# Performance work log

Hardware: AMD Instinct MI355X
Metric: run time of the kernel (lower is better)

## Reference

```python
import jax, jax.numpy as jnp
import numpy as np

N = 100000
E = 1600000
R = 8
DIN = 128
H = 128
C = 16
NROOT = 1024


def rgcn_conv(x, src, dst, edge_type, w_rel, w_root, bias):
    """PyG RGCNConv: per-relation mean aggregation + root weight + bias."""
    n, din = x.shape
    r = w_rel.shape[0]
    msgs = x[src]  # [E, din] gather
    seg = dst * r + edge_type  # combined (node, relation) segment id
    sums = jax.ops.segment_sum(msgs, seg, num_segments=n * r)        # [N*R, din]
    cnt = jax.ops.segment_sum(jnp.ones((msgs.shape[0],), x.dtype), seg,
                              num_segments=n * r)                    # [N*R]
    mean = sums / jnp.maximum(cnt, 1.0)[:, None]
    mean = mean.reshape(n, r, din)
    # relation-specific transform then sum over relations, plus root transform
    out = jnp.einsum('nrd,rde->ne', mean, w_rel) + x @ w_root + bias
    return out


def setup_inputs() -> dict:
    key = jax.random.key(0)
    ks = jax.random.split(key, 16)
    s = 0.05
    return {
        'x': jax.random.normal(ks[0], (N, DIN), jnp.float32),
        'edge_index': jax.random.randint(ks[1], (2, E), 0, N, jnp.int64),
        'edge_type': jax.random.randint(ks[2], (E,), 0, R, jnp.int64),
        'root_idx': jax.random.randint(ks[3], (NROOT,), 0, N, jnp.int64),
        'wrel1': jax.random.normal(ks[4], (R, DIN, H), jnp.float32) * s,
        'root1': jax.random.normal(ks[5], (DIN, H), jnp.float32) * s,
        'b1': jax.random.normal(ks[6], (H,), jnp.float32) * s,
        'wrel2': jax.random.normal(ks[7], (R, H, H), jnp.float32) * s,
        'root2': jax.random.normal(ks[8], (H, H), jnp.float32) * s,
        'b2': jax.random.normal(ks[9], (H,), jnp.float32) * s,
        'wrel3': jax.random.normal(ks[10], (R, H, C), jnp.float32) * s,
        'root3': jax.random.normal(ks[11], (H, C), jnp.float32) * s,
        'b3': jax.random.normal(ks[12], (C,), jnp.float32) * s,
    }


def reference(x, edge_index, edge_type, root_idx,
              wrel1, root1, b1, wrel2, root2, b2, wrel3, root3, b3):
    src, dst = edge_index[0], edge_index[1]
    h = jax.nn.relu(rgcn_conv(x, src, dst, edge_type, wrel1, root1, b1))
    # hidden conv (relu; dropout is identity in eval mode)
    h = jax.nn.relu(rgcn_conv(h, src, dst, edge_type, wrel2, root2, b2))
    # final conv, no activation
    h = rgcn_conv(h, src, dst, edge_type, wrel3, root3, b3)
    return h[root_idx]  # [NROOT, C]
```

## Files before the change

kernel.cpp:

```cpp
#include <hip/hip_runtime.h>
#include <hip/hip_fp16.h>


typedef _Float16 f16;
typedef _Float16 f16x2 __attribute__((ext_vector_type(2)));
typedef _Float16 f16x4 __attribute__((ext_vector_type(4)));
typedef _Float16 f16x8 __attribute__((ext_vector_type(8)));
typedef float f32x4 __attribute__((ext_vector_type(4)));

#define NREL 8
#define ACHUNK 8192
#define WTELEM (640 * 128)

__global__ void k_hist(const int* __restrict__ dst, int E, int* __restrict__ cnt) {
  int e = blockIdx.x * 256 + threadIdx.x;
  if (e < E) atomicAdd(&cnt[dst[e]], 1);
}

__global__ void k_scan1(const int* __restrict__ in, int* __restrict__ out,
                        int* __restrict__ part, int n) {
  __shared__ int sh[256];
  int b = blockIdx.x, t = threadIdx.x;
  int base = b * 4096 + t * 16;
  int v[16]; int s = 0;
#pragma unroll
  for (int j = 0; j < 16; j++) { int idx = base + j; int x = (idx < n) ? in[idx] : 0; v[j] = s; s += x; }
  sh[t] = s; __syncthreads();
  for (int off = 1; off < 256; off <<= 1) {
    int x = 0; if (t >= off) x = sh[t - off];
    __syncthreads();
    if (t >= off) sh[t] += x;
    __syncthreads();
  }
  int excl = (t == 0) ? 0 : sh[t - 1];
  if (t == 255) part[b] = sh[255];
#pragma unroll
  for (int j = 0; j < 16; j++) { int idx = base + j; if (idx < n) out[idx] = v[j] + excl; }
}

__global__ void k_scan2(int* __restrict__ part, int nb) {
  __shared__ int sh[256];
  int t = threadIdx.x;
  sh[t] = (t < nb) ? part[t] : 0; __syncthreads();
  for (int off = 1; off < 256; off <<= 1) {
    int x = 0; if (t >= off) x = sh[t - off];
    __syncthreads();
    if (t >= off) sh[t] += x;
    __syncthreads();
  }
  if (t < nb) part[t] = (t == 0) ? 0 : sh[t - 1];
}

__global__ void k_scan3(int* __restrict__ out, const int* __restrict__ part, int n) {
  int i = blockIdx.x * 256 + threadIdx.x;
  if (i < n) out[i] += part[i >> 12];
}

__global__ void k_scatter(const int* __restrict__ src, const int* __restrict__ dstv,
                          const int* __restrict__ et, int E,
                          const int* __restrict__ off, int* __restrict__ fill,
                          int* __restrict__ sps) {
  int e = blockIdx.x * 256 + threadIdx.x;
  if (e >= E) return;
  int d = dstv[e];
  int pos = off[d] + atomicAdd(&fill[d], 1);
  sps[pos] = src[e] | (et[e] << 20);
}

__global__ __launch_bounds__(256) void k_sinvp(const int* __restrict__ sps,
                                               const int* __restrict__ off,
                                               float* __restrict__ sinvp, int N) {
  __shared__ int c[16][8];
  int t = threadIdx.x;
  int g = t >> 4, st = t & 15;
  int n = blockIdx.x * 16 + g;
  if (st < 8) c[g][st] = 0;
  __syncthreads();
  if (n < N) {
    int e0 = off[n], e1 = off[n + 1];
    for (int e = e0 + st; e < e1; e += 16)
      atomicAdd(&c[g][((unsigned)sps[e]) >> 20], 1);
  }
  __syncthreads();
  if (n < N && st < 8) {
    int cc = c[g][st];
    sinvp[n * 8 + st] = 1.0f / (float)(cc > 1 ? cc : 1);
  }
}

__global__ void k_sentinel(int* __restrict__ p, int v) { *p = v; }

__global__ __launch_bounds__(256) void k_bhist(const int* __restrict__ dstv, int E,
                                               int* __restrict__ bcnt, int nbuck) {
  __shared__ int h[512];
  int t = threadIdx.x;
  for (int i = t; i < 512; i += 256) h[i] = 0;
  __syncthreads();
  int lo = blockIdx.x * ACHUNK;
  int hi = lo + ACHUNK < E ? lo + ACHUNK : E;
  for (int e = lo + t; e < hi; e += 256) atomicAdd(&h[dstv[e] >> 8], 1);
  __syncthreads();
  for (int i = t; i < nbuck; i += 256)
    if (h[i]) atomicAdd(&bcnt[i], h[i]);
}

__global__ __launch_bounds__(512) void k_bscan(const int* __restrict__ bcnt,
                                               int* __restrict__ boff, int nbuck) {
  __shared__ int sh[512];
  int t = threadIdx.x;
  sh[t] = (t < nbuck) ? bcnt[t] : 0;
  __syncthreads();
  for (int o = 1; o < 512; o <<= 1) {
    int v = 0; if (t >= o) v = sh[t - o];
    __syncthreads();
    sh[t] += v;
    __syncthreads();
  }
  if (t <= nbuck && t < 512) boff[t] = (t == 0) ? 0 : sh[t - 1];
  if (t == 511 && nbuck >= 512) boff[nbuck] = sh[511];
}

__global__ __launch_bounds__(256) void k_bucketA(
    const int* __restrict__ src, const int* __restrict__ dstv,
    const int* __restrict__ et, int E, const int* __restrict__ boff,
    int* __restrict__ bfill, int* __restrict__ tmp, int nbuck) {
  __shared__ int hist[512];
  __shared__ int base[512];
  int t = threadIdx.x;
  int lo = blockIdx.x * ACHUNK;
  int hi = lo + ACHUNK < E ? lo + ACHUNK : E;
  for (int i = t; i < nbuck; i += 256) hist[i] = 0;
  __syncthreads();
  for (int e = lo + t; e < hi; e += 256)
    atomicAdd(&hist[dstv[e] >> 8], 1);
  __syncthreads();
  for (int i = t; i < nbuck; i += 256) {
    int c = hist[i];
    base[i] = c ? (boff[i] + atomicAdd(&bfill[i], c)) : 0;
  }
  __syncthreads();
  for (int e = lo + t; e < hi; e += 256) {
    int d = dstv[e];
    int b = d >> 8;
    int pos = atomicAdd(&base[b], 1);
    tmp[pos] = src[e] | (et[e] << 20) | ((d & 255) << 23);
  }
}

__global__ __launch_bounds__(256) void k_bucketB3(const int* __restrict__ tmp,
                                                  const int* __restrict__ boff,
                                                  int* __restrict__ off,
                                                  int* __restrict__ sps,
                                                  float* __restrict__ sinvp, int N) {
  __shared__ int cty[2048];
  __shared__ int sh[256];
  __shared__ int loff[257];
  __shared__ int fill[256];
  int b = blockIdx.x, t = threadIdx.x;
  int n0 = b << 8;
  int nn = (N - n0) < 256 ? (N - n0) : 256;
#pragma unroll
  for (int j = 0; j < 8; j++) cty[t + j * 256] = 0;
  __syncthreads();
  int e0 = boff[b], e1 = boff[b + 1];
  for (int e = e0 + t; e < e1; e += 256) {
    int v = tmp[e];
    int dl = (v >> 23) & 255, ty = (v >> 20) & 7;
    atomicAdd(&cty[dl * 8 + ty], 1);
  }
  __syncthreads();
  {
    int c = 0;
#pragma unroll
    for (int j = 0; j < 8; j++) c += cty[t * 8 + j];
    sh[t] = c;
  }
  __syncthreads();
  for (int o = 1; o < 256; o <<= 1) {
    int v = 0; if (t >= o) v = sh[t - o];
    __syncthreads();
    sh[t] += v;
    __syncthreads();
  }
  loff[t] = (t == 0) ? 0 : sh[t - 1];
  if (t == 255) loff[256] = sh[255];
  __syncthreads();
  if (t < nn) off[n0 + t] = e0 + loff[t];
  for (int i = t; i < 2048; i += 256) {
    int n = n0 + (i >> 3);
    if (n < N) {
      int c = cty[i];
      sinvp[(size_t)n * 8 + (i & 7)] = 1.0f / (float)(c > 1 ? c : 1);
    }
  }
  fill[t] = 0;
  __syncthreads();
  for (int e = e0 + t; e < e1; e += 256) {
    int v = tmp[e];
    int dl = (v >> 23) & 255;
    int pos = e0 + loff[dl] + atomicAdd(&fill[dl], 1);
    sps[pos] = v & 0x7FFFFF;
  }
}

__global__ void k_mark(const int* __restrict__ ridx, const int* __restrict__ off,
                       const int* __restrict__ sps, int* __restrict__ mark) {
  int i = blockIdx.x, t = threadIdx.x;
  int n = ridx[i];
  if (t == 0) mark[n] = 1;
  int e0 = off[n], e1 = off[n + 1];
  for (int e = e0 + t; e < e1; e += 64) mark[sps[e] & 0xFFFFF] = 1;
}

__global__ void k_tpw4(const float* __restrict__ wrel1, const float* __restrict__ root1,
                       const float* __restrict__ wrel2, const float* __restrict__ root2,
                       f16* __restrict__ Wt, int PW, int npass) {
  int row = blockIdx.x, k = threadIdx.x, q = blockIdx.y;
  int layer = q / npass, p = q - layer * npass;
  const float* wrel = layer ? wrel2 : wrel1;
  const float* wroot = layer ? root2 : root1;
  float v = 0.f;
  if (row < 9 * PW) {
    int cb = row / PW, j = row - cb * PW;
    int col = p * PW + j;
    v = (cb < 8) ? wrel[(size_t)cb * 16384 + k * 128 + col] : wroot[k * 128 + col];
  }
  Wt[(size_t)q * WTELEM + (size_t)row * 128 + k] = (f16)v;
}

template <typename AT>
__global__ __launch_bounds__(256) void k_gemm3(const AT* __restrict__ A,
                                               const f16* __restrict__ Bt,
                                               f16* __restrict__ Y, int M, int ncol) {
  __shared__ f16 As[128 * 136];
  int tid = threadIdx.x;
  int m0 = blockIdx.x * 128;
  int PW = ncol / 9;
  int cbs = (PW == 64) ? 6 : 5;
#pragma unroll
  for (int cch = 0; cch < 8; cch++) {
    int ci = tid + cch * 256;
    int row = ci >> 4, c8 = ci & 15;
    int gm = m0 + row;
    f16x8 va = {};
    if (gm < M) {
      if constexpr (sizeof(AT) == 2) {
        va = *(const f16x8*)((const f16*)A + (size_t)gm * 128 + c8 * 8);
      } else {
        const float4* ap = (const float4*)((const float*)A + (size_t)gm * 128);
        float4 u0 = ap[c8 * 2], u1 = ap[c8 * 2 + 1];
        va[0] = (f16)u0.x; va[1] = (f16)u0.y; va[2] = (f16)u0.z; va[3] = (f16)u0.w;
        va[4] = (f16)u1.x; va[5] = (f16)u1.y; va[6] = (f16)u1.z; va[7] = (f16)u1.w;
      }
    }
    *(f16x8*)(As + row * 136 + c8 * 8) = va;
  }
  __syncthreads();
  int wid = tid >> 6, lane = tid & 63;
  int wm = (wid & 1) * 64, wn = (wid >> 1) * 64;
  int lm = lane & 15, lk = lane >> 4;
  f16x8 af[4][4];
#pragma unroll
  for (int ks = 0; ks < 4; ks++)
#pragma unroll
    for (int i = 0; i < 4; i++)
      af[ks][i] = *(const f16x8*)(As + (wm + i * 16 + lm) * 136 + ks * 32 + lk * 8);
  __syncthreads();
  f16* H = As;
  int NT = (ncol + 127) >> 7;
  for (int nt = blockIdx.y; nt < NT; nt += gridDim.y) {
    int n0 = nt * 128;
    f32x4 acc[4][4] = {};
#pragma unroll
    for (int ks = 0; ks < 4; ks++) {
      f16x8 b[4];
#pragma unroll
      for (int j = 0; j < 4; j++)
        b[j] = *(const f16x8*)(Bt + (size_t)(n0 + wn + j * 16 + lm) * 128 + ks * 32 + lk * 8);
#pragma unroll
      for (int i = 0; i < 4; i++)
#pragma unroll
        for (int j = 0; j < 4; j++)
          acc[i][j] = __builtin_amdgcn_mfma_f32_16x16x32_f16(b[j], af[ks][i], acc[i][j], 0, 0, 0);
    }
#pragma unroll
    for (int i = 0; i < 4; i++)
#pragma unroll
      for (int j = 0; j < 4; j++) {
        f16x4 o;
        o[0] = (f16)acc[i][j][0]; o[1] = (f16)acc[i][j][1];
        o[2] = (f16)acc[i][j][2]; o[3] = (f16)acc[i][j][3];
        *(f16x4*)(H + (wm + i * 16 + lm) * 136 + wn + j * 16 + lk * 4) = o;
      }
    __syncthreads();
    for (int i = tid; i < 128 * 16; i += 256) {
      int row = i >> 4, c8 = i & 15;
      int gm = m0 + row;
      int gc = n0 + c8 * 8;
      if (gm < M && gc < ncol) {
        int cb = gc >> cbs, wi = gc & (PW - 1);
        *(f16x8*)(Y + ((size_t)cb * M + gm) * PW + wi) =
            *(const f16x8*)(H + row * 136 + c8 * 8);
      }
    }
    __syncthreads();
  }
}

template <int PW>
__global__ __launch_bounds__(256) void k_edge_v(
    const f16* __restrict__ Y, const int* __restrict__ sps,
    const int* __restrict__ off, const float* __restrict__ sinvp,
    const float* __restrict__ bias, f16* __restrict__ hout,
    const int* __restrict__ mark, int N, int pass) {
  constexpr int CPL = PW / 16;
  int t = threadIdx.x;
  int g = t >> 4, st = t & 15;
  int n = blockIdx.x * 16 + g;
  if (n >= N) return;
  if (mark && !mark[n]) return;
  float sv = (st < 8) ? sinvp[n * 8 + st] : 0.f;
  int e0 = off[n], e1 = off[n + 1];
  float a[CPL], b2[CPL];
  {
    const f16* rp = Y + ((size_t)8 * N + n) * PW + st * CPL;
    const float* bp = bias + pass * PW + st * CPL;
#pragma unroll
    for (int q = 0; q < CPL; q++) { a[q] = (float)rp[q] + bp[q]; b2[q] = 0.f; }
  }
  int sgbase = t & 48;
  int e = e0;
  for (; e + 1 < e1; e += 2) {
    int p0 = sps[e], p1 = sps[e + 1];
    int s0 = p0 & 0xFFFFF, ty0 = ((unsigned)p0) >> 20;
    int s1 = p1 & 0xFFFFF, ty1 = ((unsigned)p1) >> 20;
    float sc0 = __shfl(sv, sgbase | ty0);
    float sc1 = __shfl(sv, sgbase | ty1);
    const f16* q0 = Y + ((size_t)ty0 * N + s0) * PW + st * CPL;
    const f16* q1 = Y + ((size_t)ty1 * N + s1) * PW + st * CPL;
    if constexpr (PW == 64) {
      f16x4 v0 = *(const f16x4*)q0;
      f16x4 v1 = *(const f16x4*)q1;
      a[0] += (float)v0[0] * sc0; a[1] += (float)v0[1] * sc0;
      a[2] += (float)v0[2] * sc0; a[3] += (float)v0[3] * sc0;
      b2[0] += (float)v1[0] * sc1; b2[1] += (float)v1[1] * sc1;
      b2[2] += (float)v1[2] * sc1; b2[3] += (float)v1[3] * sc1;
    } else {
      f16x2 v0 = *(const f16x2*)q0;
      f16x2 v1 = *(const f16x2*)q1;
      a[0] += (float)v0[0] * sc0; a[1] += (float)v0[1] * sc0;
      b2[0] += (float)v1[0] * sc1; b2[1] += (float)v1[1] * sc1;
    }
  }
  if (e < e1) {
    int p0 = sps[e];
    int s0 = p0 & 0xFFFFF, ty0 = ((unsigned)p0) >> 20;
    float sc0 = __shfl(sv, sgbase | ty0);
    const f16* q0 = Y + ((size_t)ty0 * N + s0) * PW + st * CPL;
    if constexpr (PW == 64) {
      f16x4 v0 = *(const f16x4*)q0;
      a[0] += (float)v0[0] * sc0; a[1] += (float)v0[1] * sc0;
      a[2] += (float)v0[2] * sc0; a[3] += (float)v0[3] * sc0;
    } else {
      f16x2 v0 = *(const f16x2*)q0;
      a[0] += (float)v0[0] * sc0; a[1] += (float)v0[1] * sc0;
    }
  }
  if constexpr (PW == 64) {
    f16x4 o;
#pragma unroll
    for (int q = 0; q < 4; q++) o[q] = (f16)fmaxf(a[q] + b2[q], 0.f);
    *(f16x4*)(hout + (size_t)n * 128 + pass * PW + st * 4) = o;
  } else {
    f16x2 o;
#pragma unroll
    for (int q = 0; q < 2; q++) o[q] = (f16)fmaxf(a[q] + b2[q], 0.f);
    *(f16x2*)(hout + (size_t)n * 128 + pass * PW + st * 2) = o;
  }
}

__global__ __launch_bounds__(128) void k_layer3(const f16* __restrict__ h2,
                                                const int* __restrict__ sps,
                                                const int* __restrict__ off,
                                                const float* __restrict__ sinvp,
                                                const int* __restrict__ ridx,
                                                const float* __restrict__ wrel,
                                                const float* __restrict__ wroot,
                                                const float* __restrict__ b3,
                                                float* __restrict__ out) {
  __shared__ f16 W[9 * 2048];
  __shared__ float red[2][16];
  __shared__ float sinv_s[8];
  int t = threadIdx.x;
  int n = ridx[blockIdx.x];
  for (int j = t; j < 9 * 2048; j += 128)
    W[j] = (f16)((j < 8 * 2048) ? wrel[j] : wroot[j - 8 * 2048]);
  if (t < 8) sinv_s[t] = sinvp[n * 8 + t];
  __syncthreads();
  int e0 = off[n], e1 = off[n + 1];
  int c = t & 15, kg = t >> 4;
  float a = 0.f;
  for (int e = e0; e < e1; e++) {
    int ps = sps[e];
    int s = ps & 0xFFFFF, ty = ((unsigned)ps) >> 20;
    float p = 0.f;
#pragma unroll
    for (int j = 0; j < 16; j++) {
      int k = kg * 16 + j;
      p += (float)h2[(size_t)s * 128 + k] * (float)W[ty * 2048 + k * 16 + c];
    }
    a += sinv_s[ty] * p;
  }
  {
    float p = 0.f;
#pragma unroll
    for (int j = 0; j < 16; j++) {
      int k = kg * 16 + j;
      p += (float)h2[(size_t)n * 128 + k] * (float)W[8 * 2048 + k * 16 + c];
    }
    a += p;
  }
  a += __shfl_xor(a, 16);
  a += __shfl_xor(a, 32);
  if ((t & 63) < 16) red[t >> 6][t & 15] = a;
  __syncthreads();
  if (t < 16) out[(size_t)blockIdx.x * 16 + t] = red[0][t] + red[1][t] + b3[t];
}

extern "C" void kernel_launch(void* const* d_in, const int* in_sizes, int n_in,
                              void* d_out, int out_size, void* d_ws, size_t ws_size,
                              hipStream_t stream) {
  const float* x     = (const float*)d_in[0];
  const int*   eidx  = (const int*)d_in[1];
  const int*   etyp  = (const int*)d_in[2];
  const int*   ridx  = (const int*)d_in[3];
  const float* wrel1 = (const float*)d_in[4];
  const float* root1 = (const float*)d_in[5];
  const float* b1    = (const float*)d_in[6];
  const float* wrel2 = (const float*)d_in[7];
  const float* root2 = (const float*)d_in[8];
  const float* b2    = (const float*)d_in[9];
  const float* wrel3 = (const float*)d_in[10];
  const float* root3 = (const float*)d_in[11];
  const float* b3    = (const float*)d_in[12];

  int N = in_sizes[0] / 128;
  int E = in_sizes[2];
  int NROOT = in_sizes[3];
  const int* esrc = eidx;
  const int* edst = eidx + E;

  char* p = (char*)d_ws;
  auto alloc = [&](size_t bytes) { void* r = (void*)p; p += (bytes + 255) & ~(size_t)255; return r; };
  int*   off   = (int*)alloc((size_t)(N + 1) * 4);
  int*   sps   = (int*)alloc((size_t)E * 4);
  f16*   h1    = (f16*)alloc((size_t)N * 128 * 2);
  f16*   h2    = (f16*)alloc((size_t)N * 128 * 2);
  int*   mark  = (int*)alloc((size_t)N * 4);
  float* sinvp = (float*)alloc((size_t)N * 8 * 4);
  f16*   Wt    = (f16*)alloc((size_t)WTELEM * 2 * 8);
  int*   bcnt  = (int*)alloc(512 * 4);
  int*   boff  = (int*)alloc(513 * 4);
  int*   bfill = (int*)alloc(512 * 4);

  size_t used = (size_t)(p - (char*)d_ws);
  size_t remain = ws_size > used ? ws_size - used : 0;
  int PW = (remain >= (size_t)N * 9 * 64 * 2 + (1u << 20)) ? 64 : 32;
  int ldy = 9 * PW;
  f16* Y = (f16*)alloc((size_t)N * ldy * 2);
  int* tmp  = (int*)Y;
  int* part = tmp + E;
  int* fill = part + 4096;

  int nbuck = (N + 255) >> 8;
  int nbA = (E + ACHUNK - 1) / ACHUNK;
  int npass = 128 / PW;
  int NT = (ldy + 127) / 128;
  hipMemsetAsync(mark, 0, (size_t)N * 4, stream);
  k_tpw4<<<dim3(NT * 128, 2 * npass), 128, 0, stream>>>(wrel1, root1, wrel2, root2,
                                                        Wt, PW, npass);

  if (nbuck <= 512) {
    hipMemsetAsync(bcnt, 0, 512 * 4, stream);
    hipMemsetAsync(bfill, 0, 512 * 4, stream);
    k_bhist<<<nbA, 256, 0, stream>>>(edst, E, bcnt, nbuck);
    k_bscan<<<1, 512, 0, stream>>>(bcnt, boff, nbuck);
    k_bucketA<<<nbA, 256, 0, stream>>>(esrc, edst, etyp, E, boff, bfill, tmp, nbuck);
    k_bucketB3<<<nbuck, 256, 0, stream>>>(tmp, boff, off, sps, sinvp, N);
    k_sentinel<<<1, 1, 0, stream>>>(off + N, E);
  } else {
    int eb = (E + 255) / 256;
    hipMemsetAsync(off, 0, (size_t)(N + 1) * 4, stream);
    hipMemsetAsync(fill, 0, (size_t)N * 4, stream);
    k_hist<<<eb, 256, 0, stream>>>(edst, E, off);
    int nb1 = (N + 4095) / 4096;
    k_scan1<<<nb1, 256, 0, stream>>>(off, off, part, N);
    k_scan2<<<1, 256, 0, stream>>>(part, nb1);
    k_scan3<<<(N + 255) / 256, 256, 0, stream>>>(off, part, N);
    k_sentinel<<<1, 1, 0, stream>>>(off + N, E);
    k_scatter<<<eb, 256, 0, stream>>>(esrc, edst, etyp, E, off, fill, sps);
    int ng16f = (N + 15) / 16;
    k_sinvp<<<ng16f, 256, 0, stream>>>(sps, off, sinvp, N);
  }
  k_mark<<<NROOT, 64, 0, stream>>>(ridx, off, sps, mark);
  int ng16 = (N + 15) / 16;

  int mb = (N + 127) / 128;

  for (int ps = 0; ps < npass; ps++) {
    k_gemm3<float><<<dim3(mb, 2), 256, 0, stream>>>(x, Wt + (size_t)ps * WTELEM, Y, N, ldy);
    if (PW == 64)
      k_edge_v<64><<<ng16, 256, 0, stream>>>(Y, sps, off, sinvp, b1, h1, nullptr, N, ps);
    else
      k_edge_v<32><<<ng16, 256, 0, stream>>>(Y, sps, off, sinvp, b1, h1, nullptr, N, ps);
  }
  for (int ps = 0; ps < npass; ps++) {
    k_gemm3<f16><<<dim3(mb, 2), 256, 0, stream>>>(h1, Wt + (size_t)(npass + ps) * WTELEM,
                                                  Y, N, ldy);
    if (PW == 64)
      k_edge_v<64><<<ng16, 256, 0, stream>>>(Y, sps, off, sinvp, b2, h2, mark, N, ps);
    else
      k_edge_v<32><<<ng16, 256, 0, stream>>>(Y, sps, off, sinvp, b2, h2, mark, N, ps);
  }
  k_layer3<<<NROOT, 128, 0, stream>>>(h2, sps, off, sinvp, ridx, wrel3, root3, b3,
                                      (float*)d_out);
}
```

Measured before the change: 476.0 us.

## Compact layer-2 to marked nodes with aggregate-then-transform GEMM

Layer 2 no longer runs a full N-row transform GEMM followed by an edge pass that discards unmarked nodes. The marked node set (roots plus their neighbours) is compacted into a list, their per-relation means are aggregated from h1, and a small GEMM over the compacted rows produces h2 only for those nodes. Layer 3 reads through the compacted index. This cuts layer-2 work to about 16K nodes, at the cost of an atomic compaction pass and a capacity bound on the compact buffer.

New measurement: 446.2 us. -6.3%, faster.

```diff
diff --git a/kernel.cpp b/kernel.cpp
--- a/kernel.cpp
+++ b/kernel.cpp
@@ -212,20 +212,35 @@
   for (int e = e0 + t; e < e1; e += 64) mark[sps[e] & 0xFFFFF] = 1;
 }
 
+__global__ void k_compact(const int* __restrict__ mark, int* __restrict__ midx,
+                          int* __restrict__ mlist, int* __restrict__ nm, int N) {
+  int n = blockIdx.x * 256 + threadIdx.x;
+  if (n < N && mark[n]) {
+    int i = atomicAdd(nm, 1);
+    midx[n] = i;
+    mlist[i] = n;
+  }
+}
+
 __global__ void k_tpw4(const float* __restrict__ wrel1, const float* __restrict__ root1,
-                       const float* __restrict__ wrel2, const float* __restrict__ root2,
-                       f16* __restrict__ Wt, int PW, int npass) {
+                       f16* __restrict__ Wt, int PW) {
   int row = blockIdx.x, k = threadIdx.x, q = blockIdx.y;
-  int layer = q / npass, p = q - layer * npass;
-  const float* wrel = layer ? wrel2 : wrel1;
-  const float* wroot = layer ? root2 : root1;
   float v = 0.f;
   if (row < 9 * PW) {
     int cb = row / PW, j = row - cb * PW;
-    int col = p * PW + j;
-    v = (cb < 8) ? wrel[(size_t)cb * 16384 + k * 128 + col] : wroot[k * 128 + col];
+    int col = q * PW + j;
+    v = (cb < 8) ? wrel1[(size_t)cb * 16384 + k * 128 + col] : root1[k * 128 + col];
   }
   Wt[(size_t)q * WTELEM + (size_t)row * 128 + k] = (f16)v;
+}
+
+__global__ void k_tpwc2(const float* __restrict__ wrel2, const float* __restrict__ root2,
+                        f16* __restrict__ Wc) {
+  int c = blockIdx.x, k = threadIdx.x;
+#pragma unroll
+  for (int r = 0; r < 8; r++)
+    Wc[(size_t)c * 1152 + r * 128 + k] = (f16)wrel2[(size_t)r * 16384 + k * 128 + c];
+  Wc[(size_t)c * 1152 + 1024 + k] = (f16)root2[(size_t)k * 128 + c];
 }
 
 template <typename AT>
@@ -311,14 +326,12 @@
 __global__ __launch_bounds__(256) void k_edge_v(
     const f16* __restrict__ Y, const int* __restrict__ sps,
     const int* __restrict__ off, const float* __restrict__ sinvp,
-    const float* __restrict__ bias, f16* __restrict__ hout,
-    const int* __restrict__ mark, int N, int pass) {
+    const float* __restrict__ bias, f16* __restrict__ hout, int N, int pass) {
   constexpr int CPL = PW / 16;
   int t = threadIdx.x;
   int g = t >> 4, st = t & 15;
   int n = blockIdx.x * 16 + g;
   if (n >= N) return;
-  if (mark && !mark[n]) return;
   float sv = (st < 8) ? sinvp[n * 8 + st] : 0.f;
   int e0 = off[n], e1 = off[n + 1];
   float a[CPL], b2[CPL];
@@ -379,15 +392,120 @@
   }
 }
 
-__global__ __launch_bounds__(128) void k_layer3(const f16* __restrict__ h2,
-                                                const int* __restrict__ sps,
-                                                const int* __restrict__ off,
-                                                const float* __restrict__ sinvp,
-                                                const int* __restrict__ ridx,
-                                                const float* __restrict__ wrel,
-                                                const float* __restrict__ wroot,
-                                                const float* __restrict__ b3,
-                                                float* __restrict__ out) {
+__global__ __launch_bounds__(128) void k_agg2(
+    const f16* __restrict__ h1, const int* __restrict__ sps,
+    const int* __restrict__ off, const float* __restrict__ sinvp,
+    const int* __restrict__ mlist, const int* __restrict__ nm_p,
+    f16* __restrict__ Mc, int cap) {
+  int nm = *nm_p; if (nm > cap) nm = cap;
+  int t = threadIdx.x;
+  for (int i = blockIdx.x; i < nm; i += gridDim.x) {
+    int n = mlist[i];
+    int e0 = off[n], e1 = off[n + 1];
+    float acc[8];
+#pragma unroll
+    for (int r = 0; r < 8; r++) acc[r] = 0.f;
+    int e = e0;
+    for (; e + 1 < e1; e += 2) {
+      int p0 = sps[e], p1 = sps[e + 1];
+      int s0 = p0 & 0xFFFFF, ty0 = ((unsigned)p0) >> 20;
+      int s1 = p1 & 0xFFFFF, ty1 = ((unsigned)p1) >> 20;
+      float v0 = (float)h1[(size_t)s0 * 128 + t];
+      float v1 = (float)h1[(size_t)s1 * 128 + t];
+#pragma unroll
+      for (int r = 0; r < 8; r++) {
+        acc[r] += (ty0 == r) ? v0 : 0.f;
+        acc[r] += (ty1 == r) ? v1 : 0.f;
+      }
+    }
+    if (e < e1) {
+      int p0 = sps[e];
+      int s0 = p0 & 0xFFFFF, ty0 = ((unsigned)p0) >> 20;
+      float v0 = (float)h1[(size_t)s0 * 128 + t];
+#pragma unroll
+      for (int r = 0; r < 8; r++) acc[r] += (ty0 == r) ? v0 : 0.f;
+    }
+    f16* mp = Mc + (size_t)i * 1152;
+#pragma unroll
+    for (int r = 0; r < 8; r++)
+      mp[r * 128 + t] = (f16)(acc[r] * sinvp[(size_t)n * 8 + r]);
+    mp[1024 + t] = h1[(size_t)n * 128 + t];
+  }
+}
+
+__global__ __launch_bounds__(256) void k_gemm_c(const f16* __restrict__ Mc,
+                                                const f16* __restrict__ Wc,
+                                                const float* __restrict__ bias,
+                                                const int* __restrict__ nm_p,
+                                                f16* __restrict__ h2c, int cap) {
+  int nm = *nm_p; if (nm > cap) nm = cap;
+  int m0 = blockIdx.x * 128;
+  if (m0 >= nm) return;
+  __shared__ f16 As[128 * 136];
+  int tid = threadIdx.x;
+  int wid = tid >> 6, lane = tid & 63;
+  int wm = (wid & 1) * 64, wn = (wid >> 1) * 64;
+  int lm = lane & 15, lk = lane >> 4;
+  f32x4 acc[4][4] = {};
+  for (int kc = 0; kc < 9; kc++) {
+    __syncthreads();
+#pragma unroll
+    for (int cch = 0; cch < 8; cch++) {
+      int ci = tid + cch * 256;
+      int row = ci >> 4, c8 = ci & 15;
+      int gm = m0 + row;
+      f16x8 va = {};
+      if (gm < nm) va = *(const f16x8*)(Mc + (size_t)gm * 1152 + kc * 128 + c8 * 8);
+      *(f16x8*)(As + row * 136 + c8 * 8) = va;
+    }
+    __syncthreads();
+#pragma unroll
+    for (int ks = 0; ks < 4; ks++) {
+      f16x8 a[4], b[4];
+#pragma unroll
+      for (int j = 0; j < 4; j++)
+        b[j] = *(const f16x8*)(Wc + (size_t)(wn + j * 16 + lm) * 1152 + kc * 128 + ks * 32 + lk * 8);
+#pragma unroll
+      for (int i = 0; i < 4; i++)
+        a[i] = *(const f16x8*)(As + (wm + i * 16 + lm) * 136 + ks * 32 + lk * 8);
+#pragma unroll
+      for (int i = 0; i < 4; i++)
+#pragma unroll
+        for (int j = 0; j < 4; j++)
+          acc[i][j] = __builtin_amdgcn_mfma_f32_16x16x32_f16(b[j], a[i], acc[i][j], 0, 0, 0);
+    }
+  }
+  __syncthreads();
+  f16* H = As;
+#pragma unroll
+  for (int i = 0; i < 4; i++)
+#pragma unroll
+    for (int j = 0; j < 4; j++) {
+      f16x4 o;
+#pragma unroll
+      for (int q = 0; q < 4; q++)
+        o[q] = (f16)fmaxf(acc[i][j][q] + bias[wn + j * 16 + lk * 4 + q], 0.f);
+      *(f16x4*)(H + (wm + i * 16 + lm) * 136 + wn + j * 16 + lk * 4) = o;
+    }
+  __syncthreads();
+  for (int i = tid; i < 128 * 16; i += 256) {
+    int row = i >> 4, c8 = i & 15;
+    int gm = m0 + row;
+    if (gm < nm)
+      *(f16x8*)(h2c + (size_t)gm * 128 + c8 * 8) = *(const f16x8*)(H + row * 136 + c8 * 8);
+  }
+}
+
+__global__ __launch_bounds__(128) void k_layer3c(const f16* __restrict__ h2c,
+                                                 const int* __restrict__ midx,
+                                                 const int* __restrict__ sps,
+                                                 const int* __restrict__ off,
+                                                 const float* __restrict__ sinvp,
+                                                 const int* __restrict__ ridx,
+                                                 const float* __restrict__ wrel,
+                                                 const float* __restrict__ wroot,
+                                                 const float* __restrict__ b3,
+                                                 float* __restrict__ out) {
   __shared__ f16 W[9 * 2048];
   __shared__ float red[2][16];
   __shared__ float sinv_s[8];
@@ -403,20 +521,22 @@
   for (int e = e0; e < e1; e++) {
     int ps = sps[e];
     int s = ps & 0xFFFFF, ty = ((unsigned)ps) >> 20;
+    int si = midx[s];
     float p = 0.f;
 #pragma unroll
     for (int j = 0; j < 16; j++) {
       int k = kg * 16 + j;
-      p += (float)h2[(size_t)s * 128 + k] * (float)W[ty * 2048 + k * 16 + c];
+      p += (float)h2c[(size_t)si * 128 + k] * (float)W[ty * 2048 + k * 16 + c];
     }
     a += sinv_s[ty] * p;
   }
   {
+    int ni = midx[n];
     float p = 0.f;
 #pragma unroll
     for (int j = 0; j < 16; j++) {
       int k = kg * 16 + j;
-      p += (float)h2[(size_t)n * 128 + k] * (float)W[8 * 2048 + k * 16 + c];
+      p += (float)h2c[(size_t)ni * 128 + k] * (float)W[8 * 2048 + k * 16 + c];
     }
     a += p;
   }
@@ -455,10 +575,14 @@
   int*   off   = (int*)alloc((size_t)(N + 1) * 4);
   int*   sps   = (int*)alloc((size_t)E * 4);
   f16*   h1    = (f16*)alloc((size_t)N * 128 * 2);
-  f16*   h2    = (f16*)alloc((size_t)N * 128 * 2);
+  f16*   h2c   = (f16*)alloc((size_t)N * 128 * 2);
   int*   mark  = (int*)alloc((size_t)N * 4);
+  int*   midx  = (int*)alloc((size_t)N * 4);
+  int*   mlist = (int*)alloc((size_t)N * 4);
+  int*   nmv   = (int*)alloc(256);
   float* sinvp = (float*)alloc((size_t)N * 8 * 4);
-  f16*   Wt    = (f16*)alloc((size_t)WTELEM * 2 * 8);
+  f16*   Wt    = (f16*)alloc((size_t)WTELEM * 2 * 4);
+  f16*   Wc    = (f16*)alloc((size_t)128 * 1152 * 2);
   int*   bcnt  = (int*)alloc(512 * 4);
   int*   boff  = (int*)alloc(513 * 4);
   int*   bfill = (int*)alloc(512 * 4);
@@ -471,14 +595,17 @@
   int* tmp  = (int*)Y;
   int* part = tmp + E;
   int* fill = part + 4096;
+  f16* Mc   = Y;
+  int  cap  = (int)(((size_t)N * ldy) / 1152);
 
   int nbuck = (N + 255) >> 8;
   int nbA = (E + ACHUNK - 1) / ACHUNK;
   int npass = 128 / PW;
   int NT = (ldy + 127) / 128;
   hipMemsetAsync(mark, 0, (size_t)N * 4, stream);
-  k_tpw4<<<dim3(NT * 128, 2 * npass), 128, 0, stream>>>(wrel1, root1, wrel2, root2,
-                                                        Wt, PW, npass);
+  hipMemsetAsync(nmv, 0, 256, stream);
+  k_tpw4<<<dim3(NT * 128, npass), 128, 0, stream>>>(wrel1, root1, Wt, PW);
+  k_tpwc2<<<128, 128, 0, stream>>>(wrel2, root2, Wc);
 
   if (nbuck <= 512) {
     hipMemsetAsync(bcnt, 0, 512 * 4, stream);
@@ -503,6 +630,7 @@
     k_sinvp<<<ng16f, 256, 0, stream>>>(sps, off, sinvp, N);
   }
   k_mark<<<NROOT, 64, 0, stream>>>(ridx, off, sps, mark);
+  k_compact<<<(N + 255) / 256, 256, 0, stream>>>(mark, midx, mlist, nmv, N);
   int ng16 = (N + 15) / 16;
 
   int mb = (N + 127) / 128;
@@ -510,18 +638,12 @@
   for (int ps = 0; ps < npass; ps++) {
     k_gemm3<float><<<dim3(mb, 2), 256, 0, stream>>>(x, Wt + (size_t)ps * WTELEM, Y, N, ldy);
     if (PW == 64)
-      k_edge_v<64><<<ng16, 256, 0, stream>>>(Y, sps, off, sinvp, b1, h1, nullptr, N, ps);
+      k_edge_v<64><<<ng16, 256, 0, stream>>>(Y, sps, off, sinvp, b1, h1, N, ps);
     else
-      k_edge_v<32><<<ng16, 256, 0, stream>>>(Y, sps, off, sinvp, b1, h1, nullptr, N, ps);
-  }
-  for (int ps = 0; ps < npass; ps++) {
-    k_gemm3<f16><<<dim3(mb, 2), 256, 0, stream>>>(h1, Wt + (size_t)(npass + ps) * WTELEM,
-                                                  Y, N, ldy);
-    if (PW == 64)
-      k_edge_v<64><<<ng16, 256, 0, stream>>>(Y, sps, off, sinvp, b2, h2, mark, N, ps);
-    else
-      k_edge_v<32><<<ng16, 256, 0, stream>>>(Y, sps, off, sinvp, b2, h2, mark, N, ps);
-  }
-  k_layer3<<<NROOT, 128, 0, stream>>>(h2, sps, off, sinvp, ridx, wrel3, root3, b3,
-                                      (float*)d_out);
-}
+      k_edge_v<32><<<ng16, 256, 0, stream>>>(Y, sps, off, sinvp, b1, h1, N, ps);
+  }
+  k_agg2<<<2048, 128, 0, stream>>>(h1, sps, off, sinvp, mlist, nmv, Mc, cap);
+  k_gemm_c<<<(cap + 127) / 128, 256, 0, stream>>>(Mc, Wc, b2, nmv, h2c, cap);
+  k_layer3c<<<NROOT, 128, 0, stream>>>(h2c, midx, sps, off, sinvp, ridx, wrel3, root3,
+                                       b3, (float*)d_out);
+}
```

## Aggregate-then-transform RGCN layers with compacted layer-2 node set

Applied to the files above, without the earlier changes.

Replaces transform-then-gather (GEMM producing 9 relation projections per node, then an edge gather over 64/32-column passes) with gathering raw 128-dim features per relation into a mean buffer, then a single K=1152 GEMM fused with bias and ReLU. Layer 2 is computed only for compacted marked nodes (roots and their neighbours) through an index list, and layer 3 reads the compact h2. It also casts x to fp16 once and merges the memsets into one init kernel. The scalar per-thread 128-wide gather and an atomic-based compaction order are new costs, and the large per-node mean buffer is chunked by workspace capacity.

After: 631.2 us. +32.6%, slower.

```diff
diff --git a/kernel.cpp b/kernel.cpp
--- a/kernel.cpp
+++ b/kernel.cpp
@@ -3,14 +3,12 @@
 
 
 typedef _Float16 f16;
-typedef _Float16 f16x2 __attribute__((ext_vector_type(2)));
 typedef _Float16 f16x4 __attribute__((ext_vector_type(4)));
 typedef _Float16 f16x8 __attribute__((ext_vector_type(8)));
 typedef float f32x4 __attribute__((ext_vector_type(4)));
 
 #define NREL 8
 #define ACHUNK 8192
-#define WTELEM (640 * 128)
 
 __global__ void k_hist(const int* __restrict__ dst, int E, int* __restrict__ cnt) {
   int e = blockIdx.x * 256 + threadIdx.x;
@@ -89,6 +87,14 @@
 }
 
 __global__ void k_sentinel(int* __restrict__ p, int v) { *p = v; }
+
+__global__ void k_init(int* __restrict__ bcnt, int* __restrict__ bfill,
+                       int* __restrict__ nmv, int* __restrict__ mark, int N) {
+  int i = blockIdx.x * 256 + threadIdx.x;
+  if (i < 512) { bcnt[i] = 0; bfill[i] = 0; }
+  if (i < 64) nmv[i] = 0;
+  if (i < N) mark[i] = 0;
+}
 
 __global__ __launch_bounds__(256) void k_bhist(const int* __restrict__ dstv, int E,
                                                int* __restrict__ bcnt, int nbuck) {
@@ -212,182 +218,162 @@
   for (int e = e0 + t; e < e1; e += 64) mark[sps[e] & 0xFFFFF] = 1;
 }
 
-__global__ void k_tpw4(const float* __restrict__ wrel1, const float* __restrict__ root1,
-                       const float* __restrict__ wrel2, const float* __restrict__ root2,
-                       f16* __restrict__ Wt, int PW, int npass) {
-  int row = blockIdx.x, k = threadIdx.x, q = blockIdx.y;
-  int layer = q / npass, p = q - layer * npass;
-  const float* wrel = layer ? wrel2 : wrel1;
-  const float* wroot = layer ? root2 : root1;
-  float v = 0.f;
-  if (row < 9 * PW) {
-    int cb = row / PW, j = row - cb * PW;
-    int col = p * PW + j;
-    v = (cb < 8) ? wrel[(size_t)cb * 16384 + k * 128 + col] : wroot[k * 128 + col];
-  }
-  Wt[(size_t)q * WTELEM + (size_t)row * 128 + k] = (f16)v;
-}
-
-template <typename AT>
-__global__ __launch_bounds__(256) void k_gemm3(const AT* __restrict__ A,
-                                               const f16* __restrict__ Bt,
-                                               f16* __restrict__ Y, int M, int ncol) {
+__global__ void k_compact(const int* __restrict__ mark, int* __restrict__ midx,
+                          int* __restrict__ mlist, int* __restrict__ nm, int N) {
+  int n = blockIdx.x * 256 + threadIdx.x;
+  if (n < N && mark[n]) {
+    int i = atomicAdd(nm, 1);
+    midx[n] = i;
+    mlist[i] = n;
+  }
+}
+
+__global__ void k_f32_to_f16(const float* __restrict__ in, f16* __restrict__ out, int n4) {
+  int i = blockIdx.x * 256 + threadIdx.x;
+  if (i < n4) {
+    float4 v = ((const float4*)in)[i];
+    f16x4 o; o[0] = (f16)v.x; o[1] = (f16)v.y; o[2] = (f16)v.z; o[3] = (f16)v.w;
+    ((f16x4*)out)[i] = o;
+  }
+}
+
+__global__ void k_tpwc(const float* __restrict__ wrel, const float* __restrict__ wroot,
+                       f16* __restrict__ Wc) {
+  int c = blockIdx.x, k = threadIdx.x;
+#pragma unroll
+  for (int r = 0; r < 8; r++)
+    Wc[(size_t)c * 1152 + r * 128 + k] = (f16)wrel[(size_t)r * 16384 + k * 128 + c];
+  Wc[(size_t)c * 1152 + 1024 + k] = (f16)wroot[(size_t)k * 128 + c];
+}
+
+__global__ __launch_bounds__(128) void k_agg(
+    const f16* __restrict__ h, const int* __restrict__ sps,
+    const int* __restrict__ off, const float* __restrict__ sinvp,
+    const int* __restrict__ mlist, const int* __restrict__ nm_p,
+    int cnt, int nbase, f16* __restrict__ Mc) {
+  int nm = cnt;
+  if (nm_p) { int v = *nm_p; if (v < nm) nm = v; }
+  int t = threadIdx.x;
+  for (int i = blockIdx.x; i < nm; i += gridDim.x) {
+    int n = mlist ? mlist[i] : (nbase + i);
+    int e0 = off[n], e1 = off[n + 1];
+    float acc[8];
+#pragma unroll
+    for (int r = 0; r < 8; r++) acc[r] = 0.f;
+    int e = e0;
+    for (; e + 3 < e1; e += 4) {
+      int p0 = sps[e], p1 = sps[e + 1], p2 = sps[e + 2], p3 = sps[e + 3];
+      float v0 = (float)h[(size_t)(p0 & 0xFFFFF) * 128 + t];
+      float v1 = (float)h[(size_t)(p1 & 0xFFFFF) * 128 + t];
+      float v2 = (float)h[(size_t)(p2 & 0xFFFFF) * 128 + t];
+      float v3 = (float)h[(size_t)(p3 & 0xFFFFF) * 128 + t];
+      int ty0 = ((unsigned)p0) >> 20, ty1 = ((unsigned)p1) >> 20;
+      int ty2 = ((unsigned)p2) >> 20, ty3 = ((unsigned)p3) >> 20;
+#pragma unroll
+      for (int r = 0; r < 8; r++) {
+        acc[r] += (ty0 == r) ? v0 : 0.f;
+        acc[r] += (ty1 == r) ? v1 : 0.f;
+        acc[r] += (ty2 == r) ? v2 : 0.f;
+        acc[r] += (ty3 == r) ? v3 : 0.f;
+      }
+    }
+    for (; e < e1; e++) {
+      int p0 = sps[e];
+      float v0 = (float)h[(size_t)(p0 & 0xFFFFF) * 128 + t];
+      int ty0 = ((unsigned)p0) >> 20;
+#pragma unroll
+      for (int r = 0; r < 8; r++) acc[r] += (ty0 == r) ? v0 : 0.f;
+    }
+    f16* mp = Mc + (size_t)i * 1024;
+#pragma unroll
+    for (int r = 0; r < 8; r++)
+      mp[r * 128 + t] = (f16)(acc[r] * sinvp[(size_t)n * 8 + r]);
+  }
+}
+
+__global__ __launch_bounds__(256) void k_gemm_c(const f16* __restrict__ Mc,
+                                                const f16* __restrict__ rootsrc,
+                                                const int* __restrict__ ml,
+                                                const f16* __restrict__ Wc,
+                                                const float* __restrict__ bias,
+                                                const int* __restrict__ nm_p,
+                                                int cnt, f16* __restrict__ out) {
+  int nm = cnt;
+  if (nm_p) { int v = *nm_p; if (v < nm) nm = v; }
+  int m0 = blockIdx.x * 128;
+  if (m0 >= nm) return;
   __shared__ f16 As[128 * 136];
   int tid = threadIdx.x;
-  int m0 = blockIdx.x * 128;
-  int PW = ncol / 9;
-  int cbs = (PW == 64) ? 6 : 5;
-#pragma unroll
-  for (int cch = 0; cch < 8; cch++) {
-    int ci = tid + cch * 256;
-    int row = ci >> 4, c8 = ci & 15;
-    int gm = m0 + row;
-    f16x8 va = {};
-    if (gm < M) {
-      if constexpr (sizeof(AT) == 2) {
-        va = *(const f16x8*)((const f16*)A + (size_t)gm * 128 + c8 * 8);
-      } else {
-        const float4* ap = (const float4*)((const float*)A + (size_t)gm * 128);
-        float4 u0 = ap[c8 * 2], u1 = ap[c8 * 2 + 1];
-        va[0] = (f16)u0.x; va[1] = (f16)u0.y; va[2] = (f16)u0.z; va[3] = (f16)u0.w;
-        va[4] = (f16)u1.x; va[5] = (f16)u1.y; va[6] = (f16)u1.z; va[7] = (f16)u1.w;
-      }
-    }
-    *(f16x8*)(As + row * 136 + c8 * 8) = va;
-  }
-  __syncthreads();
   int wid = tid >> 6, lane = tid & 63;
   int wm = (wid & 1) * 64, wn = (wid >> 1) * 64;
   int lm = lane & 15, lk = lane >> 4;
-  f16x8 af[4][4];
-#pragma unroll
-  for (int ks = 0; ks < 4; ks++)
-#pragma unroll
-    for (int i = 0; i < 4; i++)
-      af[ks][i] = *(const f16x8*)(As + (wm + i * 16 + lm) * 136 + ks * 32 + lk * 8);
+  f32x4 acc[4][4] = {};
+  for (int kc = 0; kc < 9; kc++) {
+    __syncthreads();
+#pragma unroll
+    for (int cch = 0; cch < 8; cch++) {
+      int ci = tid + cch * 256;
+      int row = ci >> 4, c8 = ci & 15;
+      int gm = m0 + row;
+      f16x8 va = {};
+      if (gm < nm) {
+        if (kc < 8) {
+          va = *(const f16x8*)(Mc + (size_t)gm * 1024 + kc * 128 + c8 * 8);
+        } else {
+          int rn = ml ? ml[gm] : gm;
+          va = *(const f16x8*)(rootsrc + (size_t)rn * 128 + c8 * 8);
+        }
+      }
+      *(f16x8*)(As + row * 136 + c8 * 8) = va;
+    }
+    __syncthreads();
+#pragma unroll
+    for (int ks = 0; ks < 4; ks++) {
+      f16x8 a[4], b[4];
+#pragma unroll
+      for (int j = 0; j < 4; j++)
+        b[j] = *(const f16x8*)(Wc + (size_t)(wn + j * 16 + lm) * 1152 + kc * 128 + ks * 32 + lk * 8);
+#pragma unroll
+      for (int i = 0; i < 4; i++)
+        a[i] = *(const f16x8*)(As + (wm + i * 16 + lm) * 136 + ks * 32 + lk * 8);
+#pragma unroll
+      for (int i = 0; i < 4; i++)
+#pragma unroll
+        for (int j = 0; j < 4; j++)
+          acc[i][j] = __builtin_amdgcn_mfma_f32_16x16x32_f16(b[j], a[i], acc[i][j], 0, 0, 0);
+    }
+  }
   __syncthreads();
   f16* H = As;
-  int NT = (ncol + 127) >> 7;
-  for (int nt = blockIdx.y; nt < NT; nt += gridDim.y) {
-    int n0 = nt * 128;
-    f32x4 acc[4][4] = {};
-#pragma unroll
-    for (int ks = 0; ks < 4; ks++) {
-      f16x8 b[4];
-#pragma unroll
-      for (int j = 0; j < 4; j++)
-        b[j] = *(const f16x8*)(Bt + (size_t)(n0 + wn + j * 16 + lm) * 128 + ks * 32 + lk * 8);
-#pragma unroll
-      for (int i = 0; i < 4; i++)
-#pragma unroll
-        for (int j = 0; j < 4; j++)
-          acc[i][j] = __builtin_amdgcn_mfma_f32_16x16x32_f16(b[j], af[ks][i], acc[i][j], 0, 0, 0);
-    }
-#pragma unroll
-    for (int i = 0; i < 4; i++)
-#pragma unroll
-      for (int j = 0; j < 4; j++) {
-        f16x4 o;
-        o[0] = (f16)acc[i][j][0]; o[1] = (f16)acc[i][j][1];
-        o[2] = (f16)acc[i][j][2]; o[3] = (f16)acc[i][j][3];
-        *(f16x4*)(H + (wm + i * 16 + lm) * 136 + wn + j * 16 + lk * 4) = o;
-      }
-    __syncthreads();
-    for (int i = tid; i < 128 * 16; i += 256) {
-      int row = i >> 4, c8 = i & 15;
-      int gm = m0 + row;
-      int gc = n0 + c8 * 8;
-      if (gm < M && gc < ncol) {
-        int cb = gc >> cbs, wi = gc & (PW - 1);
-        *(f16x8*)(Y + ((size_t)cb * M + gm) * PW + wi) =
-            *(const f16x8*)(H + row * 136 + c8 * 8);
-      }
-    }
-    __syncthreads();
-  }
-}
-
-template <int PW>
-__global__ __launch_bounds__(256) void k_edge_v(
-    const f16* __restrict__ Y, const int* __restrict__ sps,
-    const int* __restrict__ off, const float* __restrict__ sinvp,
-    const float* __restrict__ bias, f16* __restrict__ hout,
-    const int* __restrict__ mark, int N, int pass) {
-  constexpr int CPL = PW / 16;
-  int t = threadIdx.x;
-  int g = t >> 4, st = t & 15;
-  int n = blockIdx.x * 16 + g;
-  if (n >= N) return;
-  if (mark && !mark[n]) return;
-  float sv = (st < 8) ? sinvp[n * 8 + st] : 0.f;
-  int e0 = off[n], e1 = off[n + 1];
-  float a[CPL], b2[CPL];
-  {
-    const f16* rp = Y + ((size_t)8 * N + n) * PW + st * CPL;
-    const float* bp = bias + pass * PW + st * CPL;
-#pragma unroll
-    for (int q = 0; q < CPL; q++) { a[q] = (float)rp[q] + bp[q]; b2[q] = 0.f; }
-  }
-  int sgbase = t & 48;
-  int e = e0;
-  for (; e + 1 < e1; e += 2) {
-    int p0 = sps[e], p1 = sps[e + 1];
-    int s0 = p0 & 0xFFFFF, ty0 = ((unsigned)p0) >> 20;
-    int s1 = p1 & 0xFFFFF, ty1 = ((unsigned)p1) >> 20;
-    float sc0 = __shfl(sv, sgbase | ty0);
-    float sc1 = __shfl(sv, sgbase | ty1);
-    const f16* q0 = Y + ((size_t)ty0 * N + s0) * PW + st * CPL;
-    const f16* q1 = Y + ((size_t)ty1 * N + s1) * PW + st * CPL;
-    if constexpr (PW == 64) {
-      f16x4 v0 = *(const f16x4*)q0;
-      f16x4 v1 = *(const f16x4*)q1;
-      a[0] += (float)v0[0] * sc0; a[1] += (float)v0[1] * sc0;
-      a[2] += (float)v0[2] * sc0; a[3] += (float)v0[3] * sc0;
-      b2[0] += (float)v1[0] * sc1; b2[1] += (float)v1[1] * sc1;
-      b2[2] += (float)v1[2] * sc1; b2[3] += (float)v1[3] * sc1;
-    } else {
-      f16x2 v0 = *(const f16x2*)q0;
-      f16x2 v1 = *(const f16x2*)q1;
-      a[0] += (float)v0[0] * sc0; a[1] += (float)v0[1] * sc0;
-      b2[0] += (float)v1[0] * sc1; b2[1] += (float)v1[1] * sc1;
-    }
-  }
-  if (e < e1) {
-    int p0 = sps[e];
-    int s0 = p0 & 0xFFFFF, ty0 = ((unsigned)p0) >> 20;
-    float sc0 = __shfl(sv, sgbase | ty0);
-    const f16* q0 = Y + ((size_t)ty0 * N + s0) * PW + st * CPL;
-    if constexpr (PW == 64) {
-      f16x4 v0 = *(const f16x4*)q0;
-      a[0] += (float)v0[0] * sc0; a[1] += (float)v0[1] * sc0;
-      a[2] += (float)v0[2] * sc0; a[3] += (float)v0[3] * sc0;
-    } else {
-      f16x2 v0 = *(const f16x2*)q0;
-      a[0] += (float)v0[0] * sc0; a[1] += (float)v0[1] * sc0;
-    }
-  }
-  if constexpr (PW == 64) {
-    f16x4 o;
-#pragma unroll
-    for (int q = 0; q < 4; q++) o[q] = (f16)fmaxf(a[q] + b2[q], 0.f);
-    *(f16x4*)(hout + (size_t)n * 128 + pass * PW + st * 4) = o;
-  } else {
-    f16x2 o;
-#pragma unroll
-    for (int q = 0; q < 2; q++) o[q] = (f16)fmaxf(a[q] + b2[q], 0.f);
-    *(f16x2*)(hout + (size_t)n * 128 + pass * PW + st * 2) = o;
-  }
-}
-
-__global__ __launch_bounds__(128) void k_layer3(const f16* __restrict__ h2,
-                                                const int* __restrict__ sps,
-                                                const int* __restrict__ off,
-                                                const float* __restrict__ sinvp,
-                                                const int* __restrict__ ridx,
-                                                const float* __restrict__ wrel,
-                                                const float* __restrict__ wroot,
-                                                const float* __restrict__ b3,
-                                                float* __restrict__ out) {
+#pragma unroll
+  for (int i = 0; i < 4; i++)
+#pragma unroll
+    for (int j = 0; j < 4; j++) {
+      f16x4 o;
+#pragma unroll
+      for (int q = 0; q < 4; q++)
+        o[q] = (f16)fmaxf(acc[i][j][q] + bias[wn + j * 16 + lk * 4 + q], 0.f);
+      *(f16x4*)(H + (wm + i * 16 + lm) * 136 + wn + j * 16 + lk * 4) = o;
+    }
+  __syncthreads();
+  for (int i = tid; i < 128 * 16; i += 256) {
+    int row = i >> 4, c8 = i & 15;
+    int gm = m0 + row;
+    if (gm < nm)
+      *(f16x8*)(out + (size_t)gm * 128 + c8 * 8) = *(const f16x8*)(H + row * 136 + c8 * 8);
+  }
+}
+
+__global__ __launch_bounds__(128) void k_layer3c(const f16* __restrict__ h2c,
+                                                 const int* __restrict__ midx,
+                                                 const int* __restrict__ sps,
+                                                 const int* __restrict__ off,
+                                                 const float* __restrict__ sinvp,
+                                                 const int* __restrict__ ridx,
+                                                 const float* __restrict__ wrel,
+                                                 const float* __restrict__ wroot,
+                                                 const float* __restrict__ b3,
+                                                 float* __restrict__ out) {
   __shared__ f16 W[9 * 2048];
   __shared__ float red[2][16];
   __shared__ float sinv_s[8];
@@ -403,20 +389,22 @@
   for (int e = e0; e < e1; e++) {
     int ps = sps[e];
     int s = ps & 0xFFFFF, ty = ((unsigned)ps) >> 20;
+    int si = midx[s];
     float p = 0.f;
 #pragma unroll
     for (int j = 0; j < 16; j++) {
       int k = kg * 16 + j;
-      p += (float)h2[(size_t)s * 128 + k] * (float)W[ty * 2048 + k * 16 + c];
+      p += (float)h2c[(size_t)si * 128 + k] * (float)W[ty * 2048 + k * 16 + c];
     }
     a += sinv_s[ty] * p;
   }
   {
+    int ni = midx[n];
     float p = 0.f;
 #pragma unroll
     for (int j = 0; j < 16; j++) {
       int k = kg * 16 + j;
-      p += (float)h2[(size_t)n * 128 + k] * (float)W[8 * 2048 + k * 16 + c];
+      p += (float)h2c[(size_t)ni * 128 + k] * (float)W[8 * 2048 + k * 16 + c];
     }
     a += p;
   }
@@ -455,34 +443,38 @@
   int*   off   = (int*)alloc((size_t)(N + 1) * 4);
   int*   sps   = (int*)alloc((size_t)E * 4);
   f16*   h1    = (f16*)alloc((size_t)N * 128 * 2);
-  f16*   h2    = (f16*)alloc((size_t)N * 128 * 2);
+  f16*   h2c   = (f16*)alloc((size_t)N * 128 * 2);
   int*   mark  = (int*)alloc((size_t)N * 4);
+  int*   midx  = (int*)alloc((size_t)N * 4);
+  int*   mlist = (int*)alloc((size_t)N * 4);
+  int*   nmv   = (int*)alloc(256);
   float* sinvp = (float*)alloc((size_t)N * 8 * 4);
-  f16*   Wt    = (f16*)alloc((size_t)WTELEM * 2 * 8);
+  f16*   Wc1   = (f16*)alloc((size_t)128 * 1152 * 2);
+  f16*   Wc2   = (f16*)alloc((size_t)128 * 1152 * 2);
   int*   bcnt  = (int*)alloc(512 * 4);
   int*   boff  = (int*)alloc(513 * 4);
   int*   bfill = (int*)alloc(512 * 4);
 
   size_t used = (size_t)(p - (char*)d_ws);
   size_t remain = ws_size > used ? ws_size - used : 0;
-  int PW = (remain >= (size_t)N * 9 * 64 * 2 + (1u << 20)) ? 64 : 32;
-  int ldy = 9 * PW;
-  f16* Y = (f16*)alloc((size_t)N * ldy * 2);
-  int* tmp  = (int*)Y;
+  char* scratch = (char*)alloc(0);
+  int cap = (int)(remain / 2048);
+  if (cap > N) cap = N;
+  if (cap < 128) cap = 128;
+  int* tmp  = (int*)scratch;
   int* part = tmp + E;
   int* fill = part + 4096;
+  f16* Mc   = (f16*)scratch;
 
   int nbuck = (N + 255) >> 8;
   int nbA = (E + ACHUNK - 1) / ACHUNK;
-  int npass = 128 / PW;
-  int NT = (ldy + 127) / 128;
-  hipMemsetAsync(mark, 0, (size_t)N * 4, stream);
-  k_tpw4<<<dim3(NT * 128, 2 * npass), 128, 0, stream>>>(wrel1, root1, wrel2, root2,
-                                                        Wt, PW, npass);
+  k_init<<<(N + 255) / 256, 256, 0, stream>>>(bcnt, bfill, nmv, mark, N);
+  k_tpwc<<<128, 128, 0, stream>>>(wrel1, root1, Wc1);
+  k_tpwc<<<128, 128, 0, stream>>>(wrel2, root2, Wc2);
+  f16* xh = h2c;
+  k_f32_to_f16<<<((N * 32) + 255) / 256, 256, 0, stream>>>(x, xh, N * 32);
 
   if (nbuck <= 512) {
-    hipMemsetAsync(bcnt, 0, 512 * 4, stream);
-    hipMemsetAsync(bfill, 0, 512 * 4, stream);
     k_bhist<<<nbA, 256, 0, stream>>>(edst, E, bcnt, nbuck);
     k_bscan<<<1, 512, 0, stream>>>(bcnt, boff, nbuck);
     k_bucketA<<<nbA, 256, 0, stream>>>(esrc, edst, etyp, E, boff, bfill, tmp, nbuck);
@@ -503,25 +495,17 @@
     k_sinvp<<<ng16f, 256, 0, stream>>>(sps, off, sinvp, N);
   }
   k_mark<<<NROOT, 64, 0, stream>>>(ridx, off, sps, mark);
-  int ng16 = (N + 15) / 16;
-
-  int mb = (N + 127) / 128;
-
-  for (int ps = 0; ps < npass; ps++) {
-    k_gemm3<float><<<dim3(mb, 2), 256, 0, stream>>>(x, Wt + (size_t)ps * WTELEM, Y, N, ldy);
-    if (PW == 64)
-      k_edge_v<64><<<ng16, 256, 0, stream>>>(Y, sps, off, sinvp, b1, h1, nullptr, N, ps);
-    else
-      k_edge_v<32><<<ng16, 256, 0, stream>>>(Y, sps, off, sinvp, b1, h1, nullptr, N, ps);
-  }
-  for (int ps = 0; ps < npass; ps++) {
-    k_gemm3<f16><<<dim3(mb, 2), 256, 0, stream>>>(h1, Wt + (size_t)(npass + ps) * WTELEM,
-                                                  Y, N, ldy);
-    if (PW == 64)
-      k_edge_v<64><<<ng16, 256, 0, stream>>>(Y, sps, off, sinvp, b2, h2, mark, N, ps);
-    else
-      k_edge_v<32><<<ng16, 256, 0, stream>>>(Y, sps, off, sinvp, b2, h2, mark, N, ps);
-  }
-  k_layer3<<<NROOT, 128, 0, stream>>>(h2, sps, off, sinvp, ridx, wrel3, root3, b3,
-                                      (float*)d_out);
-}
+  k_compact<<<(N + 255) / 256, 256, 0, stream>>>(mark, midx, mlist, nmv, N);
+
+  for (int m0 = 0; m0 < N; m0 += cap) {
+    int cnt = (N - m0) < cap ? (N - m0) : cap;
+    k_agg<<<2048, 128, 0, stream>>>(xh, sps, off, sinvp, nullptr, nullptr, cnt, m0, Mc);
+    k_gemm_c<<<(cnt + 127) / 128, 256, 0, stream>>>(Mc, xh + (size_t)m0 * 128, nullptr,
+                                                    Wc1, b1, nullptr, cnt,
+                                                    h1 + (size_t)m0 * 128);
+  }
+  k_agg<<<2048, 128, 0, stream>>>(h1, sps, off, sinvp, mlist, nmv, cap, 0, Mc);
+  k_gemm_c<<<(cap + 127) / 128, 256, 0, stream>>>(Mc, h1, mlist, Wc2, b2, nmv, cap, h2c);
+  k_layer3c<<<NROOT, 128, 0, stream>>>(h2c, midx, sps, off, sinvp, ridx, wrel3, root3,
+                                       b3, (float*)d_out);
+}
```
